# Kernel optimization log

Hardware: AMD Instinct MI355X
Metric: run time of the kernel (lower is better)

The kernel has to match this reference:

```python
import jax, jax.numpy as jnp
import numpy as np

IN_DIM = 128
OUT_DIM = 128
DEGREE = 3
BATCH = 8192


def setup_inputs() -> dict:
    key = jax.random.key(0)
    k1, k2 = jax.random.split(key)
    x = jax.random.normal(k1, (BATCH, IN_DIM), dtype=jnp.float32)
    # coeff ~ 0.1*randn, shape [out_dim*in_dim, degree+1]
    coeff = 0.1 * jax.random.normal(k2, (OUT_DIM * IN_DIM, DEGREE + 1), dtype=jnp.float32)
    return {"x": x, "coeff": coeff}


def reference(x, coeff):
    # x: [B, in_dim], coeff: [out_dim*in_dim, D+1]
    # Original tiles x to [out_dim*in_dim, B]; edge i = (o*in_dim + j) uses x[:, j].
    # out[i,b] = sum_d coeff[i,d] * x[b, i % in_dim]**d, then sum over in_dim.
    B, in_dim = x.shape
    D1 = coeff.shape[-1]
    out_dim = coeff.shape[0] // in_dim
    exps = jnp.arange(D1, dtype=x.dtype)
    powed = x[:, :, None] ** exps            # [B, in_dim, D+1]
    c = coeff.reshape(out_dim, in_dim, D1)    # [out_dim, in_dim, D+1]
    # per-edge polynomial eval fused with sum over in_dim
    y = jnp.einsum('bid,oid->bo', powed, c)   # [B, out_dim]
    return y
```

## Files before the change

kernel.cpp:

```cpp
#include <hip/hip_runtime.h>


#define BATCH   8192
#define IN_DIM  128
#define OUT_DIM 128
#define KDIM    512
#define M_BLK   32
#define N_BLK   64
#define BK      64
#define LDSS    72

typedef __attribute__((ext_vector_type(8))) short bf16x8;
typedef __attribute__((ext_vector_type(4))) float f32x4;
typedef __attribute__((ext_vector_type(8))) unsigned short u16x8;

__device__ inline unsigned short f2bf(float f) {
    union { float f; unsigned int u; } v; v.f = f;
    unsigned int u = v.u;
    u += 0x7FFFu + ((u >> 16) & 1u);
    return (unsigned short)(u >> 16);
}

__global__ __launch_bounds__(256) void kan_mfma(const float* __restrict__ x,
                                                const float* __restrict__ coeff,
                                                float* __restrict__ out) {
    __shared__ __align__(16) unsigned short A_lds[M_BLK * LDSS];
    __shared__ __align__(16) unsigned short W_lds[N_BLK * LDSS];

    const int t    = threadIdx.x;
    const int w    = t >> 6;
    const int lane = t & 63;
    const int quad = lane >> 4;
    const int lr   = lane & 15;
    const int m0   = blockIdx.x * M_BLK;
    const int n0   = blockIdx.y * N_BLK;

    f32x4 acc0 = {0.f, 0.f, 0.f, 0.f};
    f32x4 acc1 = {0.f, 0.f, 0.f, 0.f};

    const int am  = t >> 3;
    const int ajp = t & 7;
    const int wn    = t >> 2;
    const int wpart = t & 3;

    for (int stage = 0; stage < KDIM / BK; ++stage) {
        const int k0 = stage * BK;
        const int j0 = k0 >> 2;

        const float2 xv = *(const float2*)&x[(m0 + am) * IN_DIM + j0 + ajp * 2];
        const float* cbase = &coeff[(n0 + wn) * KDIM + k0 + wpart * 16];
        const float4 c0 = *(const float4*)(cbase + 0);
        const float4 c1 = *(const float4*)(cbase + 4);
        const float4 c2 = *(const float4*)(cbase + 8);
        const float4 c3 = *(const float4*)(cbase + 12);

        __syncthreads();

        {
            u16x8 av;
            const float xa = xv.x, xb = xv.y;
            av[0] = 0x3F80u;      av[1] = f2bf(xa);
            av[2] = f2bf(xa*xa);  av[3] = f2bf(xa*xa*xa);
            av[4] = 0x3F80u;      av[5] = f2bf(xb);
            av[6] = f2bf(xb*xb);  av[7] = f2bf(xb*xb*xb);
            *(u16x8*)&A_lds[am * LDSS + ajp * 8] = av;
        }
        {
            u16x8 wv0, wv1;
            wv0[0]=f2bf(c0.x); wv0[1]=f2bf(c0.y); wv0[2]=f2bf(c0.z); wv0[3]=f2bf(c0.w);
            wv0[4]=f2bf(c1.x); wv0[5]=f2bf(c1.y); wv0[6]=f2bf(c1.z); wv0[7]=f2bf(c1.w);
            wv1[0]=f2bf(c2.x); wv1[1]=f2bf(c2.y); wv1[2]=f2bf(c2.z); wv1[3]=f2bf(c2.w);
            wv1[4]=f2bf(c3.x); wv1[5]=f2bf(c3.y); wv1[6]=f2bf(c3.z); wv1[7]=f2bf(c3.w);
            *(u16x8*)&W_lds[wn * LDSS + wpart * 16 + 0] = wv0;
            *(u16x8*)&W_lds[wn * LDSS + wpart * 16 + 8] = wv1;
        }
        __syncthreads();

        #pragma unroll
        for (int s = 0; s < 2; ++s) {
            const int ko = s * 32 + quad * 8;
            const bf16x8 a0 = *(const bf16x8*)&A_lds[lr        * LDSS + ko];
            const bf16x8 a1 = *(const bf16x8*)&A_lds[(16 + lr) * LDSS + ko];
            const bf16x8 bm = *(const bf16x8*)&W_lds[(w*16+lr) * LDSS + ko];
            acc0 = __builtin_amdgcn_mfma_f32_16x16x32_bf16(a0, bm, acc0, 0, 0, 0);
            acc1 = __builtin_amdgcn_mfma_f32_16x16x32_bf16(a1, bm, acc1, 0, 0, 0);
        }
    }

    const int col = n0 + w * 16 + lr;
    #pragma unroll
    for (int r = 0; r < 4; ++r) {
        out[(m0 +      quad * 4 + r) * OUT_DIM + col] = acc0[r];
        out[(m0 + 16 + quad * 4 + r) * OUT_DIM + col] = acc1[r];
    }
}

extern "C" void kernel_launch(void* const* d_in, const int* in_sizes, int n_in,
                              void* d_out, int out_size, void* d_ws, size_t ws_size,
                              hipStream_t stream) {
    const float* x     = (const float*)d_in[0];
    const float* coeff = (const float*)d_in[1];
    float* out = (float*)d_out;

    dim3 grid(BATCH / M_BLK, OUT_DIM / N_BLK);
    kan_mfma<<<grid, 256, 0, stream>>>(x, coeff, out);
}
```

Measured before the change: 65.06 us.

## Pre-convert coefficients to bf16 in a prep kernel and drop LDS staging

Adds a separate prep kernel that converts the fp32 coefficients to packed bf16 once into workspace. The main kernel becomes a single-wave 16x16 tile that reads bf16 weights and x straight from global memory into MFMA operands, with no LDS and no barriers. It uses the hardware packed bf16 convert when available. The cost is a second launch, smaller tiles with more blocks, and repeated global reads of x and weights per tile instead of LDS reuse.

```diff
diff --git a/kernel.cpp b/kernel.cpp
--- a/kernel.cpp
+++ b/kernel.cpp
@@ -5,14 +5,9 @@
 #define IN_DIM  128
 #define OUT_DIM 128
 #define KDIM    512
-#define M_BLK   32
-#define N_BLK   64
-#define BK      64
-#define LDSS    72
 
 typedef __attribute__((ext_vector_type(8))) short bf16x8;
 typedef __attribute__((ext_vector_type(4))) float f32x4;
-typedef __attribute__((ext_vector_type(8))) unsigned short u16x8;
 
 __device__ inline unsigned short f2bf(float f) {
     union { float f; unsigned int u; } v; v.f = f;
@@ -21,77 +16,67 @@
     return (unsigned short)(u >> 16);
 }
 
-__global__ __launch_bounds__(256) void kan_mfma(const float* __restrict__ x,
-                                                const float* __restrict__ coeff,
-                                                float* __restrict__ out) {
-    __shared__ __align__(16) unsigned short A_lds[M_BLK * LDSS];
-    __shared__ __align__(16) unsigned short W_lds[N_BLK * LDSS];
+#if defined(__has_builtin)
+#if __has_builtin(__builtin_amdgcn_cvt_pk_bf16_f32)
+#define HAVE_HW_PKBF16 1
+#endif
+#endif
 
-    const int t    = threadIdx.x;
-    const int w    = t >> 6;
-    const int lane = t & 63;
-    const int quad = lane >> 4;
-    const int lr   = lane & 15;
-    const int m0   = blockIdx.x * M_BLK;
-    const int n0   = blockIdx.y * N_BLK;
+#ifdef HAVE_HW_PKBF16
+typedef __attribute__((ext_vector_type(2))) __bf16 bf16x2_t;
+__device__ inline unsigned int pk2(float a, float b) {
+    bf16x2_t r = __builtin_amdgcn_cvt_pk_bf16_f32(a, b);
+    union { bf16x2_t v; unsigned int u; } c; c.v = r; return c.u;
+}
+#else
+__device__ inline unsigned int pk2(float a, float b) {
+    return (unsigned int)f2bf(a) | ((unsigned int)f2bf(b) << 16);
+}
+#endif
 
-    f32x4 acc0 = {0.f, 0.f, 0.f, 0.f};
-    f32x4 acc1 = {0.f, 0.f, 0.f, 0.f};
+__global__ __launch_bounds__(256) void kan_prep(const float* __restrict__ coeff,
+                                                unsigned int* __restrict__ wbf) {
+    const int i = (blockIdx.x * 256 + threadIdx.x) * 4;
+    const float4 c = *(const float4*)(coeff + i);
+    uint2 o;
+    o.x = pk2(c.x, c.y);
+    o.y = pk2(c.z, c.w);
+    *(uint2*)(wbf + i / 2) = o;
+}
 
-    const int am  = t >> 3;
-    const int ajp = t & 7;
-    const int wn    = t >> 2;
-    const int wpart = t & 3;
+__global__ __launch_bounds__(64) void kan_mfma(const float* __restrict__ x,
+                                               const unsigned short* __restrict__ wbf,
+                                               float* __restrict__ out) {
+    const int lane = threadIdx.x;
+    const int q    = lane >> 4;
+    const int r    = lane & 15;
+    const int m0   = blockIdx.x * 16;
+    const int n0   = blockIdx.y * 16;
 
-    for (int stage = 0; stage < KDIM / BK; ++stage) {
-        const int k0 = stage * BK;
-        const int j0 = k0 >> 2;
+    const float*          xrow = x   + (size_t)(m0 + r) * IN_DIM;
+    const unsigned short* wrow = wbf + (size_t)(n0 + r) * KDIM;
 
-        const float2 xv = *(const float2*)&x[(m0 + am) * IN_DIM + j0 + ajp * 2];
-        const float* cbase = &coeff[(n0 + wn) * KDIM + k0 + wpart * 16];
-        const float4 c0 = *(const float4*)(cbase + 0);
-        const float4 c1 = *(const float4*)(cbase + 4);
-        const float4 c2 = *(const float4*)(cbase + 8);
-        const float4 c3 = *(const float4*)(cbase + 12);
+    f32x4 acc = {0.f, 0.f, 0.f, 0.f};
 
-        __syncthreads();
+    #pragma unroll
+    for (int s = 0; s < KDIM / 32; ++s) {
+        const bf16x8 bw = *(const bf16x8*)(wrow + s * 32 + q * 8);
 
-        {
-            u16x8 av;
-            const float xa = xv.x, xb = xv.y;
-            av[0] = 0x3F80u;      av[1] = f2bf(xa);
-            av[2] = f2bf(xa*xa);  av[3] = f2bf(xa*xa*xa);
-            av[4] = 0x3F80u;      av[5] = f2bf(xb);
-            av[6] = f2bf(xb*xb);  av[7] = f2bf(xb*xb*xb);
-            *(u16x8*)&A_lds[am * LDSS + ajp * 8] = av;
-        }
-        {
-            u16x8 wv0, wv1;
-            wv0[0]=f2bf(c0.x); wv0[1]=f2bf(c0.y); wv0[2]=f2bf(c0.z); wv0[3]=f2bf(c0.w);
-            wv0[4]=f2bf(c1.x); wv0[5]=f2bf(c1.y); wv0[6]=f2bf(c1.z); wv0[7]=f2bf(c1.w);
-            wv1[0]=f2bf(c2.x); wv1[1]=f2bf(c2.y); wv1[2]=f2bf(c2.z); wv1[3]=f2bf(c2.w);
-            wv1[4]=f2bf(c3.x); wv1[5]=f2bf(c3.y); wv1[6]=f2bf(c3.z); wv1[7]=f2bf(c3.w);
-            *(u16x8*)&W_lds[wn * LDSS + wpart * 16 + 0] = wv0;
-            *(u16x8*)&W_lds[wn * LDSS + wpart * 16 + 8] = wv1;
-        }
-        __syncthreads();
+        const float2 xv = *(const float2*)(xrow + s * 8 + q * 2);
+        const float x0 = xv.x, x1 = xv.y;
+        union { unsigned int u[4]; bf16x8 v; } af;
+        af.u[0] = pk2(1.0f, x0);
+        af.u[1] = pk2(x0 * x0, x0 * x0 * x0);
+        af.u[2] = pk2(1.0f, x1);
+        af.u[3] = pk2(x1 * x1, x1 * x1 * x1);
 
-        #pragma unroll
-        for (int s = 0; s < 2; ++s) {
-            const int ko = s * 32 + quad * 8;
-            const bf16x8 a0 = *(const bf16x8*)&A_lds[lr        * LDSS + ko];
-            const bf16x8 a1 = *(const bf16x8*)&A_lds[(16 + lr) * LDSS + ko];
-            const bf16x8 bm = *(const bf16x8*)&W_lds[(w*16+lr) * LDSS + ko];
-            acc0 = __builtin_amdgcn_mfma_f32_16x16x32_bf16(a0, bm, acc0, 0, 0, 0);
-            acc1 = __builtin_amdgcn_mfma_f32_16x16x32_bf16(a1, bm, acc1, 0, 0, 0);
-        }
+        acc = __builtin_amdgcn_mfma_f32_16x16x32_bf16(af.v, bw, acc, 0, 0, 0);
     }
 
-    const int col = n0 + w * 16 + lr;
+    float* orow = out + (size_t)(m0 + q * 4) * OUT_DIM + n0 + r;
     #pragma unroll
-    for (int r = 0; r < 4; ++r) {
-        out[(m0 +      quad * 4 + r) * OUT_DIM + col] = acc0[r];
-        out[(m0 + 16 + quad * 4 + r) * OUT_DIM + col] = acc1[r];
+    for (int rr = 0; rr < 4; ++rr) {
+        orow[rr * OUT_DIM] = acc[rr];
     }
 }
 
@@ -102,6 +87,10 @@
     const float* coeff = (const float*)d_in[1];
     float* out = (float*)d_out;
 
-    dim3 grid(BATCH / M_BLK, OUT_DIM / N_BLK);
-    kan_mfma<<<grid, 256, 0, stream>>>(x, coeff, out);
+    unsigned int* wbf = (unsigned int*)d_ws;
+
+    kan_prep<<<OUT_DIM * KDIM / (256 * 4), 256, 0, stream>>>(coeff, wbf);
+
+    dim3 grid(BATCH / 16, OUT_DIM / 16);
+    kan_mfma<<<grid, 64, 0, stream>>>(x, (const unsigned short*)wbf, out);
 }
```

Result: slower. 72.21 us (+11.0%).
